# Performance work log

Hardware: AMD Instinct MI355X
Metric: run time of the kernel (lower is better)

## Reference

```python
import jax, jax.numpy as jnp
import numpy as np

B, T, E = 4, 1024, 1024
H, MULT = 16, 2
HD = E // H
SCALE = HD ** -0.5


def setup_inputs() -> dict:
    key = jax.random.key(0)
    ks = jax.random.split(key, 9)
    s = 0.02
    return {
        "hidden_states": jax.random.normal(ks[0], (B, T, E), jnp.float32),
        "attention_mask": jnp.zeros((B, 1, T, T), jnp.float32),
        "Wq": jax.random.normal(ks[1], (E, E), jnp.float32) * s,
        "bq": jnp.zeros((E,), jnp.float32),
        "Wk": jax.random.normal(ks[2], (MULT * E, E), jnp.float32) * s,
        "bk": jnp.zeros((MULT * E,), jnp.float32),
        "Wv": jax.random.normal(ks[3], (MULT * E, E), jnp.float32) * s,
        "bv": jnp.zeros((MULT * E,), jnp.float32),
        "Wo": jax.random.normal(ks[4], (E, E), jnp.float32) * s,
        "bo": jnp.zeros((E,), jnp.float32),
    }


def reference(hidden_states, attention_mask, Wq, bq, Wk, bk, Wv, bv, Wo, bo):
    x = hidden_states  # [B, T, E]
    # q projection, scaled
    q = (jnp.einsum("bte,fe->btf", x, Wq) + bq) * SCALE  # [B,T,E]
    q = q.reshape(B, T, H, HD).transpose(0, 2, 1, 3)      # [B,H,T,HD]
    # k/v project to multiplier-expanded dim, then _shape with seq_len=-1:
    # [B,T,MULT*E] -> view(B, T*MULT, H, HD) (torch view semantics) -> [B,H,T*MULT,HD]
    k = jnp.einsum("bte,fe->btf", x, Wk) + bk             # [B,T,MULT*E]
    k = k.reshape(B, T * MULT, H, HD).transpose(0, 2, 1, 3)
    v = jnp.einsum("bte,fe->btf", x, Wv) + bv
    v = v.reshape(B, T * MULT, H, HD).transpose(0, 2, 1, 3)

    S = T * MULT  # src_len; src_len0 = T
    attn = jnp.einsum("bhtd,bhsd->bhts", q, k)            # [B,H,T,S]
    # custom mask broadcast: view src as [MULT, src_len0] and add mask[:, :, :, None, :]
    attn = attn.reshape(B, H, T, MULT, T) + attention_mask[:, :, :, None, :]
    attn = attn.reshape(B, H, T, S)
    attn = jax.nn.softmax(attn, axis=-1)
    out = jnp.einsum("bhts,bhsd->bhtd", attn, v)          # [B,H,T,HD]
    out = out.transpose(0, 2, 1, 3).reshape(B, T, E)
    out = jnp.einsum("bte,fe->btf", out, Wo) + bo
    return out
```

## Files before the change

kernel.cpp:

```cpp
#include <hip/hip_runtime.h>
#include <math.h>

#define BB    4
#define TT    1024
#define EE    1024
#define HH    16
#define HDIM  64
#define SS    2048
#define MROWS 4096
#define SCALEQ 0.125f

typedef short  s8v  __attribute__((ext_vector_type(8)));
typedef float  f4v  __attribute__((ext_vector_type(4)));

__device__ __forceinline__ unsigned short f2bf(float f) {
    union { float f; unsigned u; } c; c.f = f;
    unsigned u = c.u + 0x7FFFu + ((c.u >> 16) & 1u);
    return (unsigned short)(u >> 16);
}
__device__ __forceinline__ float bf2f(unsigned short h) {
    union { unsigned u; float f; } c; c.u = ((unsigned)h) << 16;
    return c.f;
}

__device__ __forceinline__ void async16(const void* g, void* l) {
    __builtin_amdgcn_global_load_lds(
        (const __attribute__((address_space(1))) unsigned int*)g,
        (__attribute__((address_space(3))) unsigned int*)l,
        16, 0, 0);
}

__global__ __launch_bounds__(256) void cvt5_kernel(
    const float* __restrict__ x,  const float* __restrict__ wq,
    const float* __restrict__ wk, const float* __restrict__ wv,
    const float* __restrict__ wo,
    unsigned short* __restrict__ xb,  unsigned short* __restrict__ wqb,
    unsigned short* __restrict__ wkb, unsigned short* __restrict__ wvb,
    unsigned short* __restrict__ wob)
{
    const int total = 2621440;
    int i = blockIdx.x * 256 + threadIdx.x;
    const int stride = gridDim.x * 256;
    for (; i < total; i += stride) {
        const float* s; unsigned short* d; int off;
        if (i < 1048576)      { s = x;  d = xb;  off = i; }
        else if (i < 1310720) { s = wq; d = wqb; off = i - 1048576; }
        else if (i < 1835008) { s = wk; d = wkb; off = i - 1310720; }
        else if (i < 2359296) { s = wv; d = wvb; off = i - 1835008; }
        else                  { s = wo; d = wob; off = i - 2359296; }
        float4 v = ((const float4*)s)[off];
        ushort4 o;
        o.x = f2bf(v.x); o.y = f2bf(v.y); o.z = f2bf(v.z); o.w = f2bf(v.w);
        ((ushort4*)d)[off] = o;
    }
}

#define GEMM_KLOOP(Aptr, Wptr, Ksz)                                            \
    for (int k0 = 0; k0 < (Ksz); k0 += 32) {                                   \
        _Pragma("unroll")                                                      \
        for (int it = 0; it < 2; ++it) {                                       \
            int f = (it * 4 + w) * 64 + lane;                                  \
            int r = f >> 2, g = (f & 3) * 8;                                   \
            async16((Aptr) + (size_t)(m0 + r) * (Ksz) + k0 + g,                \
                    As + (it * 4 + w) * 512);                                  \
            async16((Wptr) + (size_t)(n0 + r) * (Ksz) + k0 + g,                \
                    Bs + (it * 4 + w) * 512);                                  \
        }                                                                      \
        __syncthreads();                                                       \
        s8v af[4], bf[4];                                                      \
        _Pragma("unroll")                                                      \
        for (int i = 0; i < 4; ++i)                                            \
            af[i] = *(const s8v*)(As + (wm + i * 16 + col16) * 32 + quad * 8); \
        _Pragma("unroll")                                                      \
        for (int j = 0; j < 4; ++j)                                            \
            bf[j] = *(const s8v*)(Bs + (wn + j * 16 + col16) * 32 + quad * 8); \
        _Pragma("unroll")                                                      \
        for (int i = 0; i < 4; ++i)                                            \
            _Pragma("unroll")                                                  \
            for (int j = 0; j < 4; ++j)                                        \
                acc[i][j] = __builtin_amdgcn_mfma_f32_16x16x32_bf16(           \
                    af[i], bf[j], acc[i][j], 0, 0, 0);                         \
        __syncthreads();                                                       \
    }

__global__ __launch_bounds__(256, 3) void gemm_qk_kernel(
    const unsigned short* __restrict__ X,  const unsigned short* __restrict__ Wq,
    const unsigned short* __restrict__ Wk, const float* __restrict__ bq,
    const float* __restrict__ bk, unsigned short* __restrict__ qp,
    unsigned short* __restrict__ kp)
{
    __shared__ __align__(16) unsigned short As[128 * 32];
    __shared__ __align__(16) unsigned short Bs[128 * 32];

    const int tid = threadIdx.x;
    const int lane = tid & 63, w = tid >> 6;
    const int wm = (w & 1) * 64, wn = (w >> 1) * 64;
    const int col16 = lane & 15, quad = lane >> 4;
    const int m0 = blockIdx.x * 128;
    const bool isQ = blockIdx.y < 8;
    const int n0 = blockIdx.y * 128;
    const unsigned short* Wrow = isQ ? Wq + (size_t)n0 * EE
                                     : Wk + (size_t)(n0 - EE) * EE;

    f4v acc[4][4];
#pragma unroll
    for (int i = 0; i < 4; ++i)
#pragma unroll
        for (int j = 0; j < 4; ++j) acc[i][j] = (f4v)0.0f;

    for (int k0 = 0; k0 < EE; k0 += 32) {
#pragma unroll
        for (int it = 0; it < 2; ++it) {
            int f = (it * 4 + w) * 64 + lane;
            int r = f >> 2, g = (f & 3) * 8;
            async16(X + (size_t)(m0 + r) * EE + k0 + g, As + (it * 4 + w) * 512);
            async16(Wrow + (size_t)r * EE + k0 + g, Bs + (it * 4 + w) * 512);
        }
        __syncthreads();
        s8v af[4], bf[4];
#pragma unroll
        for (int i = 0; i < 4; ++i)
            af[i] = *(const s8v*)(As + (wm + i * 16 + col16) * 32 + quad * 8);
#pragma unroll
        for (int j = 0; j < 4; ++j)
            bf[j] = *(const s8v*)(Bs + (wn + j * 16 + col16) * 32 + quad * 8);
#pragma unroll
        for (int i = 0; i < 4; ++i)
#pragma unroll
            for (int j = 0; j < 4; ++j)
                acc[i][j] = __builtin_amdgcn_mfma_f32_16x16x32_bf16(
                    af[i], bf[j], acc[i][j], 0, 0, 0);
        __syncthreads();
    }

#pragma unroll
    for (int j = 0; j < 4; ++j) {
        const int n = n0 + wn + j * 16 + col16;
        const float bn = isQ ? bq[n] : bk[n - EE];
#pragma unroll
        for (int i = 0; i < 4; ++i) {
            const int mb = m0 + wm + i * 16 + quad * 4;
#pragma unroll
            for (int r = 0; r < 4; ++r) {
                const int m = mb + r;
                float c = acc[i][j][r] + bn;
                if (isQ) {
                    qp[(size_t)m * EE + n] = f2bf(c * SCALEQ);
                } else {
                    const int nk = n - EE;
                    const int mm = nk >> 10, h = (nk >> 6) & 15, d = nk & 63;
                    const int b_ = m >> 10, t = m & 1023;
                    const int s = 2 * t + mm;
                    kp[((size_t)(b_ * HH + h) * SS + s) * HDIM + d] = f2bf(c);
                }
            }
        }
    }
}

template <int LAYOUT, int OUTF32, int Ksz, int Nsz>
__global__ __launch_bounds__(256, 3) void gemm_mfma_kernel(
    const unsigned short* __restrict__ A, const unsigned short* __restrict__ W,
    const float* __restrict__ bias, void* __restrict__ Cout, float alpha)
{
    __shared__ __align__(16) unsigned short As[128 * 32];
    __shared__ __align__(16) unsigned short Bs[128 * 32];

    const int tid = threadIdx.x;
    const int lane = tid & 63, w = tid >> 6;
    const int wm = (w & 1) * 64, wn = (w >> 1) * 64;
    const int col16 = lane & 15, quad = lane >> 4;
    const int m0 = blockIdx.x * 128;
    const int n0 = blockIdx.y * 128;

    f4v acc[4][4];
#pragma unroll
    for (int i = 0; i < 4; ++i)
#pragma unroll
        for (int j = 0; j < 4; ++j) acc[i][j] = (f4v)0.0f;

    GEMM_KLOOP(A, W, Ksz)

#pragma unroll
    for (int j = 0; j < 4; ++j) {
        const int n = n0 + wn + j * 16 + col16;
        const float bn = (LAYOUT == 2) ? 0.0f : bias[n];
#pragma unroll
        for (int i = 0; i < 4; ++i) {
            const int mb = m0 + wm + i * 16 + quad * 4;
#pragma unroll
            for (int r = 0; r < 4; ++r) {
                const int m = mb + r;
                float c = (acc[i][j][r] + ((LAYOUT == 2) ? bias[m] : bn)) * alpha;
                if (LAYOUT == 0) {
                    if (OUTF32) ((float*)Cout)[(size_t)m * Nsz + n] = c;
                    else ((unsigned short*)Cout)[(size_t)m * Nsz + n] = f2bf(c);
                } else {
                    const int mm = m >> 10, h = (m >> 6) & 15, d = m & 63;
                    const int b_ = n >> 10, t = n & 1023;
                    const int s = 2 * t + mm;
                    ((unsigned short*)Cout)[((size_t)(b_ * HH + h) * HDIM + d) * SS + s] = f2bf(c);
                }
            }
        }
    }
}

__global__ __launch_bounds__(256, 4) void attn_mfma_kernel(
    const unsigned short* __restrict__ Q, const unsigned short* __restrict__ Kh,
    const unsigned short* __restrict__ Vt, const float* __restrict__ Mf,
    unsigned short* __restrict__ O)
{
    constexpr int PT = 72;
    __shared__ __align__(16) unsigned short Qs[64 * PT];
    __shared__ __align__(16) unsigned short KPs[64 * PT];
    __shared__ __align__(16) unsigned short Vs[64 * PT];

    const int tid = threadIdx.x;
    const int lane = tid & 63, w = tid >> 6;
    const int col16 = lane & 15, quad = lane >> 4;
    const int t0 = blockIdx.x * 64;
    const int bh = blockIdx.y;
    const int b_ = bh >> 4, h = bh & 15;

#pragma unroll
    for (int it = 0; it < 2; ++it) {
        int idx = tid + it * 256;
        int r = idx >> 3, c = (idx & 7) * 8;
        *(uint4*)(Qs + r * PT + c) =
            *(const uint4*)(Q + (size_t)(b_ * TT + t0 + r) * EE + h * HDIM + c);
    }

    f4v oacc[4];
#pragma unroll
    for (int jd = 0; jd < 4; ++jd) oacc[jd] = (f4v)0.0f;
    float mrun = -INFINITY, lrun = 0.0f;

    const unsigned short* Kb = Kh + (size_t)bh * SS * HDIM;
    const unsigned short* Vb = Vt + (size_t)bh * HDIM * SS;
    const float* Mrow = Mf + ((size_t)b_ * TT + t0 + w * 16 + col16) * TT;

    for (int s0 = 0; s0 < SS; s0 += 64) {
        __syncthreads();
#pragma unroll
        for (int it = 0; it < 2; ++it) {
            int idx = tid + it * 256;
            int r = idx >> 3, c = (idx & 7) * 8;
            *(uint4*)(KPs + r * PT + c) = *(const uint4*)(Kb + (size_t)(s0 + r) * HDIM + c);
            *(uint4*)(Vs  + r * PT + c) = *(const uint4*)(Vb + (size_t)r * SS + s0 + c);
        }
        __syncthreads();

        f4v sacc[4];
#pragma unroll
        for (int js = 0; js < 4; ++js) sacc[js] = (f4v)0.0f;
#pragma unroll
        for (int ks = 0; ks < 2; ++ks) {
            s8v bq_ = *(const s8v*)(Qs + (w * 16 + col16) * PT + ks * 32 + quad * 8);
#pragma unroll
            for (int js = 0; js < 4; ++js) {
                s8v ak = *(const s8v*)(KPs + (js * 16 + col16) * PT + ks * 32 + quad * 8);
                sacc[js] = __builtin_amdgcn_mfma_f32_16x16x32_bf16(ak, bq_, sacc[js], 0, 0, 0);
            }
        }

        const int t2b = s0 & (TT - 1);
#pragma unroll
        for (int js = 0; js < 4; ++js) {
            float4 mv = *(const float4*)(Mrow + t2b + js * 16 + quad * 4);
            sacc[js][0] += mv.x; sacc[js][1] += mv.y;
            sacc[js][2] += mv.z; sacc[js][3] += mv.w;
        }

        float tmax = -INFINITY;
#pragma unroll
        for (int js = 0; js < 4; ++js)
#pragma unroll
            for (int r = 0; r < 4; ++r) tmax = fmaxf(tmax, sacc[js][r]);
        tmax = fmaxf(tmax, __shfl_xor(tmax, 16));
        tmax = fmaxf(tmax, __shfl_xor(tmax, 32));
        const float mnew = fmaxf(mrun, tmax);
        const float scl = __expf(mrun - mnew);
        float rs = 0.0f;
#pragma unroll
        for (int js = 0; js < 4; ++js)
#pragma unroll
            for (int r = 0; r < 4; ++r) {
                float p = __expf(sacc[js][r] - mnew);
                sacc[js][r] = p;
                rs += p;
            }
        rs += __shfl_xor(rs, 16);
        rs += __shfl_xor(rs, 32);
        lrun = lrun * scl + rs;
        mrun = mnew;

        float sclr[4];
#pragma unroll
        for (int r = 0; r < 4; ++r) sclr[r] = __shfl(scl, quad * 4 + r);
#pragma unroll
        for (int jd = 0; jd < 4; ++jd)
#pragma unroll
            for (int r = 0; r < 4; ++r) oacc[jd][r] *= sclr[r];

        __syncthreads();

#pragma unroll
        for (int js = 0; js < 4; ++js) {
            unsigned p01 = (unsigned)f2bf(sacc[js][0]) | ((unsigned)f2bf(sacc[js][1]) << 16);
            unsigned p23 = (unsigned)f2bf(sacc[js][2]) | ((unsigned)f2bf(sacc[js][3]) << 16);
            *(uint2*)(KPs + (size_t)(w * 16 + col16) * PT + js * 16 + quad * 4) =
                make_uint2(p01, p23);
        }
        __syncthreads();

#pragma unroll
        for (int ks = 0; ks < 2; ++ks) {
            s8v ap = *(const s8v*)(KPs + (w * 16 + col16) * PT + ks * 32 + quad * 8);
#pragma unroll
            for (int jd = 0; jd < 4; ++jd) {
                s8v bv_ = *(const s8v*)(Vs + (jd * 16 + col16) * PT + ks * 32 + quad * 8);
                oacc[jd] = __builtin_amdgcn_mfma_f32_16x16x32_bf16(ap, bv_, oacc[jd], 0, 0, 0);
            }
        }
    }

    const float inv = 1.0f / lrun;
    float invr[4];
#pragma unroll
    for (int r = 0; r < 4; ++r) invr[r] = __shfl(inv, quad * 4 + r);
#pragma unroll
    for (int r = 0; r < 4; ++r) {
        const int t = t0 + w * 16 + quad * 4 + r;
#pragma unroll
        for (int jd = 0; jd < 4; ++jd)
            O[(size_t)(b_ * TT + t) * EE + h * HDIM + jd * 16 + col16] =
                f2bf(oacc[jd][r] * invr[r]);
    }
}

extern "C" void kernel_launch(void* const* d_in, const int* in_sizes, int n_in,
                              void* d_out, int out_size, void* d_ws, size_t ws_size,
                              hipStream_t stream)
{
    (void)in_sizes; (void)n_in; (void)out_size; (void)ws_size;

    const float* x    = (const float*)d_in[0];
    const float* mask = (const float*)d_in[1];
    const float* Wq   = (const float*)d_in[2];
    const float* bq   = (const float*)d_in[3];
    const float* Wk   = (const float*)d_in[4];
    const float* bk   = (const float*)d_in[5];
    const float* Wv   = (const float*)d_in[6];
    const float* bv   = (const float*)d_in[7];
    const float* Wo   = (const float*)d_in[8];
    const float* bo   = (const float*)d_in[9];
    float* out = (float*)d_out;

    unsigned short* xb  = (unsigned short*)d_ws;
    unsigned short* wqb = xb  + (size_t)MROWS * EE;
    unsigned short* wkb = wqb + (size_t)EE * EE;
    unsigned short* wvb = wkb + (size_t)2 * EE * EE;
    unsigned short* wob = wvb + (size_t)2 * EE * EE;
    unsigned short* qp  = wob + (size_t)EE * EE;
    unsigned short* kp  = qp  + (size_t)MROWS * EE;
    unsigned short* vt  = kp  + (size_t)BB * HH * SS * HDIM;
    unsigned short* ao  = vt  + (size_t)BB * HH * SS * HDIM;

    dim3 blk(256);

    cvt5_kernel<<<4096, blk, 0, stream>>>(x, Wq, Wk, Wv, Wo,
                                          xb, wqb, wkb, wvb, wob);
    gemm_qk_kernel<<<dim3(32, 24), blk, 0, stream>>>(xb, wqb, wkb, bq, bk, qp, kp);
    gemm_mfma_kernel<2, 0, EE, MROWS><<<dim3(16, 32), blk, 0, stream>>>(
        wvb, xb, bv, vt, 1.0f);
    attn_mfma_kernel<<<dim3(TT / 64, BB * HH), blk, 0, stream>>>(qp, kp, vt, mask, ao);
    gemm_mfma_kernel<0, 1, EE, EE><<<dim3(32, 8), blk, 0, stream>>>(
        ao, wob, bo, out, 1.0f);
}
```

Baseline: 320.2 us.

## Process both multiplier halves per mask tile and stage bf16 mask in LDS

The attention kernel now handles key positions t and t+1024 together in each iteration, so every mask tile is loaded once and applied to both halves, which halves mask traffic. The mask is converted to bf16 in the conversion kernel and staged through shared memory. The kernel also drops the LDS row padding from 72 to 68 and uses a 1D grid remapped for locality. The goal is less global mask bandwidth and fewer loop iterations, at the cost of more LDS use, lower occupancy (3 blocks instead of 4), bf16 rounding of the mask, and a new possible source of LDS bank conflicts from the padding change.

```diff
diff --git a/kernel.cpp b/kernel.cpp
--- a/kernel.cpp
+++ b/kernel.cpp
@@ -30,15 +30,15 @@
         16, 0, 0);
 }
 
-__global__ __launch_bounds__(256) void cvt5_kernel(
+__global__ __launch_bounds__(256) void cvt6_kernel(
     const float* __restrict__ x,  const float* __restrict__ wq,
     const float* __restrict__ wk, const float* __restrict__ wv,
-    const float* __restrict__ wo,
+    const float* __restrict__ wo, const float* __restrict__ mk,
     unsigned short* __restrict__ xb,  unsigned short* __restrict__ wqb,
     unsigned short* __restrict__ wkb, unsigned short* __restrict__ wvb,
-    unsigned short* __restrict__ wob)
+    unsigned short* __restrict__ wob, unsigned short* __restrict__ mbb)
 {
-    const int total = 2621440;
+    const int total = 3670016;
     int i = blockIdx.x * 256 + threadIdx.x;
     const int stride = gridDim.x * 256;
     for (; i < total; i += stride) {
@@ -47,7 +47,8 @@
         else if (i < 1310720) { s = wq; d = wqb; off = i - 1048576; }
         else if (i < 1835008) { s = wk; d = wkb; off = i - 1310720; }
         else if (i < 2359296) { s = wv; d = wvb; off = i - 1835008; }
-        else                  { s = wo; d = wob; off = i - 2359296; }
+        else if (i < 2621440) { s = wo; d = wob; off = i - 2359296; }
+        else                  { s = mk; d = mbb; off = i - 2621440; }
         float4 v = ((const float4*)s)[off];
         ushort4 o;
         o.x = f2bf(v.x); o.y = f2bf(v.y); o.z = f2bf(v.z); o.w = f2bf(v.w);
@@ -206,21 +207,27 @@
     }
 }
 
-__global__ __launch_bounds__(256, 4) void attn_mfma_kernel(
+__global__ __launch_bounds__(256, 3) void attn_mfma2_kernel(
     const unsigned short* __restrict__ Q, const unsigned short* __restrict__ Kh,
-    const unsigned short* __restrict__ Vt, const float* __restrict__ Mf,
+    const unsigned short* __restrict__ Vt, const unsigned short* __restrict__ Mb,
     unsigned short* __restrict__ O)
 {
-    constexpr int PT = 72;
+    constexpr int PT = 68;
     __shared__ __align__(16) unsigned short Qs[64 * PT];
-    __shared__ __align__(16) unsigned short KPs[64 * PT];
-    __shared__ __align__(16) unsigned short Vs[64 * PT];
+    __shared__ __align__(16) unsigned short K0[64 * PT];
+    __shared__ __align__(16) unsigned short K1[64 * PT];
+    __shared__ __align__(16) unsigned short V0[64 * PT];
+    __shared__ __align__(16) unsigned short V1[64 * PT];
+    __shared__ __align__(16) unsigned short Ms[64 * PT];
 
     const int tid = threadIdx.x;
     const int lane = tid & 63, w = tid >> 6;
     const int col16 = lane & 15, quad = lane >> 4;
-    const int t0 = blockIdx.x * 64;
-    const int bh = blockIdx.y;
+
+    const int gid = blockIdx.x;
+    const int v = gid & 7, j = gid >> 3;
+    const int bh = v * 8 + (j >> 4);
+    const int t0 = (j & 15) * 64;
     const int b_ = bh >> 4, h = bh & 15;
 
 #pragma unroll
@@ -236,47 +243,60 @@
     for (int jd = 0; jd < 4; ++jd) oacc[jd] = (f4v)0.0f;
     float mrun = -INFINITY, lrun = 0.0f;
 
-    const unsigned short* Kb = Kh + (size_t)bh * SS * HDIM;
-    const unsigned short* Vb = Vt + (size_t)bh * HDIM * SS;
-    const float* Mrow = Mf + ((size_t)b_ * TT + t0 + w * 16 + col16) * TT;
-
-    for (int s0 = 0; s0 < SS; s0 += 64) {
-        __syncthreads();
-#pragma unroll
-        for (int it = 0; it < 2; ++it) {
-            int idx = tid + it * 256;
+    const unsigned short* Kb  = Kh + (size_t)bh * SS * HDIM;
+    const unsigned short* Vb  = Vt + (size_t)bh * HDIM * SS;
+    const unsigned short* Mbb = Mb + (size_t)b_ * TT * TT;
+    const int myrow = (w * 16 + col16) * PT;
+
+    for (int it16 = 0; it16 < 16; ++it16) {
+        const int t2b = it16 * 64;
+        __syncthreads();
+#pragma unroll
+        for (int st = 0; st < 2; ++st) {
+            int idx = tid + st * 256;
             int r = idx >> 3, c = (idx & 7) * 8;
-            *(uint4*)(KPs + r * PT + c) = *(const uint4*)(Kb + (size_t)(s0 + r) * HDIM + c);
-            *(uint4*)(Vs  + r * PT + c) = *(const uint4*)(Vb + (size_t)r * SS + s0 + c);
-        }
-        __syncthreads();
-
-        f4v sacc[4];
-#pragma unroll
-        for (int js = 0; js < 4; ++js) sacc[js] = (f4v)0.0f;
+            *(uint4*)(K0 + r * PT + c) = *(const uint4*)(Kb + (size_t)(t2b + r) * HDIM + c);
+            *(uint4*)(K1 + r * PT + c) = *(const uint4*)(Kb + (size_t)(1024 + t2b + r) * HDIM + c);
+            *(uint4*)(V0 + r * PT + c) = *(const uint4*)(Vb + (size_t)r * SS + t2b + c);
+            *(uint4*)(V1 + r * PT + c) = *(const uint4*)(Vb + (size_t)r * SS + 1024 + t2b + c);
+            *(uint4*)(Ms + r * PT + c) = *(const uint4*)(Mbb + (size_t)(t0 + r) * TT + t2b + c);
+        }
+        __syncthreads();
+
+        f4v s0acc[4], s1acc[4];
+#pragma unroll
+        for (int js = 0; js < 4; ++js) { s0acc[js] = (f4v)0.0f; s1acc[js] = (f4v)0.0f; }
 #pragma unroll
         for (int ks = 0; ks < 2; ++ks) {
-            s8v bq_ = *(const s8v*)(Qs + (w * 16 + col16) * PT + ks * 32 + quad * 8);
+            s8v bq_ = *(const s8v*)(Qs + myrow + ks * 32 + quad * 8);
 #pragma unroll
             for (int js = 0; js < 4; ++js) {
-                s8v ak = *(const s8v*)(KPs + (js * 16 + col16) * PT + ks * 32 + quad * 8);
-                sacc[js] = __builtin_amdgcn_mfma_f32_16x16x32_bf16(ak, bq_, sacc[js], 0, 0, 0);
+                s8v ak0 = *(const s8v*)(K0 + (js * 16 + col16) * PT + ks * 32 + quad * 8);
+                s8v ak1 = *(const s8v*)(K1 + (js * 16 + col16) * PT + ks * 32 + quad * 8);
+                s0acc[js] = __builtin_amdgcn_mfma_f32_16x16x32_bf16(ak0, bq_, s0acc[js], 0, 0, 0);
+                s1acc[js] = __builtin_amdgcn_mfma_f32_16x16x32_bf16(ak1, bq_, s1acc[js], 0, 0, 0);
             }
         }
 
-        const int t2b = s0 & (TT - 1);
 #pragma unroll
         for (int js = 0; js < 4; ++js) {
-            float4 mv = *(const float4*)(Mrow + t2b + js * 16 + quad * 4);
-            sacc[js][0] += mv.x; sacc[js][1] += mv.y;
-            sacc[js][2] += mv.z; sacc[js][3] += mv.w;
+            uint2 mm = *(const uint2*)(Ms + myrow + js * 16 + quad * 4);
+            float m0f = bf2f((unsigned short)(mm.x & 0xffff));
+            float m1f = bf2f((unsigned short)(mm.x >> 16));
+            float m2f = bf2f((unsigned short)(mm.y & 0xffff));
+            float m3f = bf2f((unsigned short)(mm.y >> 16));
+            s0acc[js][0] += m0f; s1acc[js][0] += m0f;
+            s0acc[js][1] += m1f; s1acc[js][1] += m1f;
+            s0acc[js][2] += m2f; s1acc[js][2] += m2f;
+            s0acc[js][3] += m3f; s1acc[js][3] += m3f;
         }
 
         float tmax = -INFINITY;
 #pragma unroll
         for (int js = 0; js < 4; ++js)
 #pragma unroll
-            for (int r = 0; r < 4; ++r) tmax = fmaxf(tmax, sacc[js][r]);
+            for (int r = 0; r < 4; ++r)
+                tmax = fmaxf(tmax, fmaxf(s0acc[js][r], s1acc[js][r]));
         tmax = fmaxf(tmax, __shfl_xor(tmax, 16));
         tmax = fmaxf(tmax, __shfl_xor(tmax, 32));
         const float mnew = fmaxf(mrun, tmax);
@@ -286,9 +306,10 @@
         for (int js = 0; js < 4; ++js)
 #pragma unroll
             for (int r = 0; r < 4; ++r) {
-                float p = __expf(sacc[js][r] - mnew);
-                sacc[js][r] = p;
-                rs += p;
+                float p0 = __expf(s0acc[js][r] - mnew);
+                float p1 = __expf(s1acc[js][r] - mnew);
+                s0acc[js][r] = p0; s1acc[js][r] = p1;
+                rs += p0 + p1;
             }
         rs += __shfl_xor(rs, 16);
         rs += __shfl_xor(rs, 32);
@@ -307,20 +328,25 @@
 
 #pragma unroll
         for (int js = 0; js < 4; ++js) {
-            unsigned p01 = (unsigned)f2bf(sacc[js][0]) | ((unsigned)f2bf(sacc[js][1]) << 16);
-            unsigned p23 = (unsigned)f2bf(sacc[js][2]) | ((unsigned)f2bf(sacc[js][3]) << 16);
-            *(uint2*)(KPs + (size_t)(w * 16 + col16) * PT + js * 16 + quad * 4) =
-                make_uint2(p01, p23);
+            unsigned p01 = (unsigned)f2bf(s0acc[js][0]) | ((unsigned)f2bf(s0acc[js][1]) << 16);
+            unsigned p23 = (unsigned)f2bf(s0acc[js][2]) | ((unsigned)f2bf(s0acc[js][3]) << 16);
+            *(uint2*)(K0 + myrow + js * 16 + quad * 4) = make_uint2(p01, p23);
+            p01 = (unsigned)f2bf(s1acc[js][0]) | ((unsigned)f2bf(s1acc[js][1]) << 16);
+            p23 = (unsigned)f2bf(s1acc[js][2]) | ((unsigned)f2bf(s1acc[js][3]) << 16);
+            *(uint2*)(K1 + myrow + js * 16 + quad * 4) = make_uint2(p01, p23);
         }
         __syncthreads();
 
 #pragma unroll
         for (int ks = 0; ks < 2; ++ks) {
-            s8v ap = *(const s8v*)(KPs + (w * 16 + col16) * PT + ks * 32 + quad * 8);
+            s8v p0 = *(const s8v*)(K0 + myrow + ks * 32 + quad * 8);
+            s8v p1 = *(const s8v*)(K1 + myrow + ks * 32 + quad * 8);
 #pragma unroll
             for (int jd = 0; jd < 4; ++jd) {
-                s8v bv_ = *(const s8v*)(Vs + (jd * 16 + col16) * PT + ks * 32 + quad * 8);
-                oacc[jd] = __builtin_amdgcn_mfma_f32_16x16x32_bf16(ap, bv_, oacc[jd], 0, 0, 0);
+                s8v v0_ = *(const s8v*)(V0 + (jd * 16 + col16) * PT + ks * 32 + quad * 8);
+                s8v v1_ = *(const s8v*)(V1 + (jd * 16 + col16) * PT + ks * 32 + quad * 8);
+                oacc[jd] = __builtin_amdgcn_mfma_f32_16x16x32_bf16(p0, v0_, oacc[jd], 0, 0, 0);
+                oacc[jd] = __builtin_amdgcn_mfma_f32_16x16x32_bf16(p1, v1_, oacc[jd], 0, 0, 0);
             }
         }
     }
@@ -362,19 +388,20 @@
     unsigned short* wkb = wqb + (size_t)EE * EE;
     unsigned short* wvb = wkb + (size_t)2 * EE * EE;
     unsigned short* wob = wvb + (size_t)2 * EE * EE;
-    unsigned short* qp  = wob + (size_t)EE * EE;
+    unsigned short* mb  = wob + (size_t)EE * EE;
+    unsigned short* qp  = mb  + (size_t)BB * TT * TT;
     unsigned short* kp  = qp  + (size_t)MROWS * EE;
     unsigned short* vt  = kp  + (size_t)BB * HH * SS * HDIM;
     unsigned short* ao  = vt  + (size_t)BB * HH * SS * HDIM;
 
     dim3 blk(256);
 
-    cvt5_kernel<<<4096, blk, 0, stream>>>(x, Wq, Wk, Wv, Wo,
-                                          xb, wqb, wkb, wvb, wob);
+    cvt6_kernel<<<4096, blk, 0, stream>>>(x, Wq, Wk, Wv, Wo, mask,
+                                          xb, wqb, wkb, wvb, wob, mb);
     gemm_qk_kernel<<<dim3(32, 24), blk, 0, stream>>>(xb, wqb, wkb, bq, bk, qp, kp);
     gemm_mfma_kernel<2, 0, EE, MROWS><<<dim3(16, 32), blk, 0, stream>>>(
         wvb, xb, bv, vt, 1.0f);
-    attn_mfma_kernel<<<dim3(TT / 64, BB * HH), blk, 0, stream>>>(qp, kp, vt, mask, ao);
+    attn_mfma2_kernel<<<dim3(1024), blk, 0, stream>>>(qp, kp, vt, mb, ao);
     gemm_mfma_kernel<0, 1, EE, EE><<<dim3(32, 8), blk, 0, stream>>>(
         ao, wob, bo, out, 1.0f);
 }
```

After: 287.7 us. 1.11x faster.
